# Kernel tuning notes

Hardware: AMD Instinct MI355X
Metric: run time of the kernel (lower is better)

The kernel has to match this reference:

```python
import jax, jax.numpy as jnp
import numpy as np

B, N, D = 128, 64, 20
H, WM = 256, 4
CAUG = D + 1                      # time-augmented path channels
SIG = CAUG + CAUG * (CAUG - 1) // 2   # depth-2 log-signature channels = 231
C = SIG + 1                       # time-augmented control channels = 232
EPS = 1e-5


def _ln(x, g, b):
    m = jnp.mean(x, -1, keepdims=True)
    v = jnp.var(x, -1, keepdims=True)
    return (x - m) * jax.lax.rsqrt(v + EPS) * g + b


def setup_inputs():
    key = jax.random.key(0)
    ks = jax.random.split(key, 12)
    w = lambda k, s: (jax.random.normal(k, s) * 0.02).astype(jnp.float32)
    z = lambda s: jnp.zeros(s, jnp.float32)
    o = lambda s: jnp.ones(s, jnp.float32)
    return dict(
        x=jax.random.normal(ks[0], (B, N, D), jnp.float32),
        hW1=w(ks[1], (D, H)), hb1=z(H), hW2=w(ks[2], (H, H)), hb2=z(H),
        fW1=w(ks[3], (H, WM * H)), fb1=z(WM * H), g1=o(WM * H), be1=z(WM * H),
        fW2=w(ks[4], (WM * H, H)), fb2=z(H), g2=o(H), be2=z(H),
        fW3=w(ks[5], (H, H)), fb3=z(H),
        fW4=w(ks[6], (H, H * C)), fb4=z(H * C),
        yW1=w(ks[7], (H, H // 2)), yb1=z(H // 2), yW2=w(ks[8], (H // 2, 1)), yb2=z(1),
        zW1=w(ks[9], (H, H)), zb1=z(H), zW2=w(ks[10], (H, D)), zb2=z(D),
        sg=o(SIG), sb=z(SIG),
    )


def _forward(x, hW1, hb1, hW2, hb2, fW1, fb1, g1, be1, fW2, fb2, g2, be2,
             fW3, fb3, fW4, fb4, yW1, yb1, yW2, yb2, zW1, zb1, zW2, zb2, sg, sb):
    t = jnp.linspace(0.0, 1.0, N).astype(x.dtype)
    # --- depth-2 streamed log-signature of time-augmented path, basepoint 0 ---
    p = jnp.concatenate([jnp.broadcast_to(t[None, :, None], (B, N, 1)), x], -1)  # (B,N,CAUG)
    prev = jnp.concatenate([jnp.zeros((B, 1, CAUG), x.dtype), p[:, :-1]], 1)
    d = p - prev                                          # piecewise-linear segment increments
    term = prev[..., :, None] * d[..., None, :] - d[..., :, None] * prev[..., None, :]
    levy = 0.5 * jnp.cumsum(term, axis=1)                 # Levy areas, (B,N,CAUG,CAUG)
    iu, ju = np.triu_indices(CAUG, 1)
    logsig = jnp.concatenate([p, levy[:, :, iu, ju]], -1)  # level-1 + level-2 log-sig, (B,N,SIG)
    logsig = _ln(logsig, sg, sb)                          # sig_norm
    # --- natural cubic spline of time-augmented control ---
    y = jnp.concatenate([jnp.broadcast_to(t[None, :, None], (B, N, 1)), logsig], -1)  # (B,N,C)
    h = 1.0 / (N - 1)
    A = np.zeros((N, N), np.float32)
    A[0, 0] = A[-1, -1] = 1.0
    for i in range(1, N - 1):
        A[i, i - 1] = h / 6.0
        A[i, i] = 2.0 * h / 3.0
        A[i, i + 1] = h / 6.0
    rhs = jnp.concatenate([jnp.zeros((B, 1, C), y.dtype),
                           (y[:, 2:] - 2.0 * y[:, 1:-1] + y[:, :-2]) / h,
                           jnp.zeros((B, 1, C), y.dtype)], 1)
    M = jnp.linalg.solve(jnp.asarray(A), rhs.transpose(1, 0, 2).reshape(N, B * C))
    M = M.reshape(N, B, C).transpose(1, 0, 2)             # natural-spline second derivatives
    dy = (y[:, 1:] - y[:, :-1]) / h
    d_knot = dy - (h / 6.0) * (2.0 * M[:, :-1] + M[:, 1:])   # dX/dt at left knots, (B,N-1,C)
    d_mid = dy + (h / 24.0) * (M[:, :-1] - M[:, 1:])         # dX/dt at segment midpoints
    # --- initial hidden state ---
    h0 = jax.nn.relu(x[:, 0] @ hW1 + hb1) @ hW2 + hb2

    def vf(zz):  # RDEFunc MLP -> (B,H,C)
        a = jax.nn.relu(_ln(zz @ fW1 + fb1, g1, be1))
        a = jax.nn.relu(_ln(a @ fW2 + fb2, g2, be2))
        a = jax.nn.relu(a @ fW3 + fb3)
        return (a @ fW4 + fb4).reshape(B, H, C)

    def g(zz, dX):
        return jnp.einsum('bhc,bc->bh', vf(zz), dX)

    def step(zz, dd):  # explicit midpoint step of dz = F(z) dX/dt dt
        dk, dm = dd
        k1 = g(zz, dk)
        zn = zz + h * g(zz + 0.5 * h * k1, dm)
        return zn, zn

    _, hs = jax.lax.scan(step, h0, (d_knot.transpose(1, 0, 2), d_mid.transpose(1, 0, 2)))
    hT = hs[-1]                                            # terminal hidden (return_path=False)
    Y = jax.nn.relu(hT @ yW1 + yb1) @ yW2 + yb2
    Z = jax.nn.relu(hT @ zW1 + zb1) @ zW2 + zb2
    return Y, Z, hT


def reference(x, hW1, hb1, hW2, hb2, fW1, fb1, g1, be1, fW2, fb2, g2, be2,
              fW3, fb3, fW4, fb4, yW1, yb1, yW2, yb2, zW1, zb1, zW2, zb2, sg, sb):
    return _forward(x, hW1, hb1, hW2, hb2, fW1, fb1, g1, be1, fW2, fb2, g2, be2,
                    fW3, fb3, fW4, fb4, yW1, yb1, yW2, yb2, zW1, zb1, zW2, zb2, sg, sb)
```

## Files before the change

kernel.cpp:

```cpp
#include <hip/hip_runtime.h>

#define B 128
#define N 64
#define D 20
#define H 256
#define WMH 1024
#define CAUG 21
#define SIG 231
#define C 232
#define CP 240
#define KA 288
#define NSEG 63
#define NPH 126
#define HSTEP (1.0f/63.0f)
#define EPS 1e-5f

typedef __attribute__((ext_vector_type(8))) short short8;
typedef __attribute__((ext_vector_type(4))) float f32x4;
typedef __attribute__((ext_vector_type(4))) unsigned int uint4v;
typedef unsigned int uint;

__device__ inline short f2bf(float f) {
  uint u = __float_as_uint(f);
  uint r = (u + 0x7fffu + ((u >> 16) & 1u)) >> 16;
  return (short)r;
}
__device__ inline float bf2f(short h) {
  return __uint_as_float(((uint)(unsigned short)h) << 16);
}
#define MFMA16(a, b, c) __builtin_amdgcn_mfma_f32_16x16x32_bf16((a), (b), (c), 0, 0, 0)

__device__ inline uint cloadu(const uint* p) {
  return __hip_atomic_load(p, __ATOMIC_RELAXED, __HIP_MEMORY_SCOPE_AGENT);
}
__device__ inline void cstoreu(uint* p, uint v) {
  __hip_atomic_store(p, v, __ATOMIC_RELAXED, __HIP_MEMORY_SCOPE_AGENT);
}
__device__ inline void cstoref(float* p, float v) {
  __hip_atomic_store(p, v, __ATOMIC_RELAXED, __HIP_MEMORY_SCOPE_AGENT);
}
__device__ inline int cloadi(const int* p) {
  return __hip_atomic_load(p, __ATOMIC_RELAXED, __HIP_MEMORY_SCOPE_AGENT);
}
__device__ inline void cstorei(int* p, int v) {
  __hip_atomic_store(p, v, __ATOMIC_RELAXED, __HIP_MEMORY_SCOPE_AGENT);
}

#define CLOAD8(r0,r1,r2,r3,r4,r5,r6,r7,addr)                                   \
  asm volatile("global_load_dwordx4 %0, %8, off sc0 sc1\n\t"                   \
               "global_load_dwordx4 %1, %8, off offset:16 sc0 sc1\n\t"         \
               "global_load_dwordx4 %2, %8, off offset:128 sc0 sc1\n\t"        \
               "global_load_dwordx4 %3, %8, off offset:144 sc0 sc1\n\t"        \
               "global_load_dwordx4 %4, %8, off offset:256 sc0 sc1\n\t"        \
               "global_load_dwordx4 %5, %8, off offset:272 sc0 sc1\n\t"        \
               "global_load_dwordx4 %6, %8, off offset:384 sc0 sc1\n\t"        \
               "global_load_dwordx4 %7, %8, off offset:400 sc0 sc1\n\t"        \
               "s_waitcnt vmcnt(0)"                                            \
               : "=&v"(r0), "=&v"(r1), "=&v"(r2), "=&v"(r3),                   \
                 "=&v"(r4), "=&v"(r5), "=&v"(r6), "=&v"(r7)                    \
               : "v"(addr)                                                     \
               : "memory")

#define CLOAD2(r0,r1,addr)                                                     \
  asm volatile("global_load_dwordx4 %0, %2, off sc0 sc1\n\t"                   \
               "global_load_dwordx4 %1, %2, off offset:16 sc0 sc1\n\t"         \
               "s_waitcnt vmcnt(0)"                                            \
               : "=&v"(r0), "=&v"(r1) : "v"(addr) : "memory")

#define CLOAD3A(r0,r1,r2,a0,a1,a2)                                             \
  asm volatile("global_load_dwordx4 %0, %3, off sc0 sc1\n\t"                   \
               "global_load_dwordx4 %1, %4, off sc0 sc1\n\t"                   \
               "global_load_dwordx4 %2, %5, off sc0 sc1\n\t"                   \
               "s_waitcnt vmcnt(0)"                                            \
               : "=&v"(r0), "=&v"(r1), "=&v"(r2)                               \
               : "v"(a0), "v"(a1), "v"(a2) : "memory")

__device__ inline void waitflag(const int* f, int v) {
  if (threadIdx.x == 0) {
    while (cloadi(f) < v) __builtin_amdgcn_s_sleep(2);
  }
  __builtin_amdgcn_fence(__ATOMIC_ACQUIRE, "workgroup");
  __syncthreads();
}
__device__ inline void siggroup(int* c, int nprod, int* flag) {
  __builtin_amdgcn_fence(__ATOMIC_RELEASE, "workgroup");
  __syncthreads();
  if (threadIdx.x == 0) {
    int old = __hip_atomic_fetch_add(c, 1, __ATOMIC_RELAXED, __HIP_MEMORY_SCOPE_AGENT);
    if (old == nprod - 1) cstorei(flag, 1);
  }
}

__device__ inline void unpk(uint4v a, uint4v b, short8& ah, short8& al) {
#pragma unroll
  for (int e = 0; e < 4; e++) {
    ah[e]     = (short)(a[e] >> 16); al[e]     = (short)(a[e] & 0xffffu);
    ah[4 + e] = (short)(b[e] >> 16); al[4 + e] = (short)(b[e] & 0xffffu);
  }
}

__global__ __launch_bounds__(256) void k_logsig(const float* __restrict__ x,
                                                const float* __restrict__ sg,
                                                const float* __restrict__ sb,
                                                float* __restrict__ y) {
  __shared__ float yb[N][C];
  int b = blockIdx.x, tid = threadIdx.x;
  for (int ii = tid; ii < N * CAUG; ii += 256) {
    int n = ii / CAUG, j = ii % CAUG;
    float v = (j == 0) ? (n * (1.0f / 63.0f)) : x[(b * N + n) * D + (j - 1)];
    yb[n][1 + j] = v;
  }
  __syncthreads();
  if (tid < 210) {
    int i = 0, rem = tid;
    while (rem >= (CAUG - 1) - i) { rem -= (CAUG - 1) - i; i++; }
    int j = i + 1 + rem;
    float acc = 0.f, pi_prev = 0.f, pj_prev = 0.f;
    for (int n = 0; n < N; n++) {
      float pi = yb[n][1 + i], pj = yb[n][1 + j];
      float di = pi - pi_prev, dj = pj - pj_prev;
      acc += 0.5f * (pi_prev * dj - di * pj_prev);
      yb[n][1 + CAUG + tid] = acc;
      pi_prev = pi; pj_prev = pj;
    }
  }
  __syncthreads();
  int w = tid >> 6, l = tid & 63;
  for (int n = w; n < N; n += 4) {
    float s1 = 0.f, s2 = 0.f;
    for (int s = l; s < SIG; s += 64) { float v = yb[n][1 + s]; s1 += v; s2 += v * v; }
    for (int off = 32; off > 0; off >>= 1) { s1 += __shfl_down(s1, off); s2 += __shfl_down(s2, off); }
    s1 = __shfl(s1, 0); s2 = __shfl(s2, 0);
    float mean = s1 * (1.0f / SIG);
    float var  = s2 * (1.0f / SIG) - mean * mean;
    float rs = rsqrtf(var + EPS);
    float* yrow = y + ((size_t)b * N + n) * C;
    if (l == 0) yrow[0] = n * (1.0f / 63.0f);
    for (int s = l; s < SIG; s += 64)
      yrow[1 + s] = (yb[n][1 + s] - mean) * rs * sg[s] + sb[s];
  }
}

__global__ __launch_bounds__(256) void k_spline(const float* __restrict__ y,
                                                float* __restrict__ dknot,
                                                float* __restrict__ dmid) {
  __shared__ float yb[N * C];
  __shared__ float cp_s[62], id_s[62];
  int b = blockIdx.x, tid = threadIdx.x;
  for (int ii = tid; ii < N * C; ii += 256) yb[ii] = y[(size_t)b * N * C + ii];
  if (tid == 0) {
    const float a = HSTEP / 6.f, bb = 2.f * HSTEP / 3.f;
    float id0 = 1.f / bb; id_s[0] = id0; cp_s[0] = a * id0;
    for (int j = 1; j < 62; j++) {
      float den = bb - a * cp_s[j - 1];
      float idj = 1.f / den; id_s[j] = idj; cp_s[j] = a * idj;
    }
  }
  __syncthreads();
  int c = tid;
  if (c >= 232 && c < CP) {
    for (int n = 0; n < NSEG; n++) {
      dknot[((size_t)n * B + b) * CP + c] = 0.f;
      dmid [((size_t)n * B + b) * CP + c] = 0.f;
    }
  } else if (c < 232) {
    const float a = HSTEP / 6.f;
    float dp[62];
    dp[0] = (yb[2 * C + c] - 2.f * yb[1 * C + c] + yb[0 * C + c]) * 63.0f * id_s[0];
#pragma unroll
    for (int j = 1; j < 62; j++) {
      float rj = (yb[(j + 2) * C + c] - 2.f * yb[(j + 1) * C + c] + yb[j * C + c]) * 63.0f;
      dp[j] = (rj - a * dp[j - 1]) * id_s[j];
    }
// ... 49 lines not shown
    int m = m0 + mloc;
    int hh = m / 232, cc = m - hh * 232;
    W4T[((size_t)hh * CP + cc) * KA + k0 + lane] = f2bf(tile[lane][mloc]);
  }
}

__global__ __launch_bounds__(256) void k_prep_pad(const float* __restrict__ fb4,
                                                  short* __restrict__ W4T) {
  int idx = blockIdx.x * 256 + threadIdx.x;
  const int partA = 61440 * 32;
  if (idx < partA) {
    int row = idx >> 5, j = idx & 31;
    int hh = row / CP, cc = row - hh * CP;
    short v = 0;
    if (j == 0 && cc < 232) v = f2bf(fb4[hh * 232 + cc]);
    W4T[(size_t)row * KA + 256 + j] = v;
  } else {
    int t = idx - partA;
    int k = t & 255; t >>= 8;
    int cc = 232 + (t & 7); int hh = t >> 3;
    W4T[((size_t)hh * CP + cc) * KA + k] = 0;
  }
}

__global__ __launch_bounds__(256) void k_prep_wt(const float* __restrict__ in,
                                                 short* __restrict__ out,
                                                 int K, int Nn) {
  __shared__ float tile[64][65];
  int n0 = blockIdx.x * 64, k0 = blockIdx.y * 64;
  int lane = threadIdx.x & 63, wr = threadIdx.x >> 6;
#pragma unroll
  for (int j = 0; j < 16; j++) {
    int kk = wr * 16 + j;
    tile[kk][lane] = in[(size_t)(k0 + kk) * Nn + n0 + lane];
  }
  __syncthreads();
#pragma unroll
  for (int j = 0; j < 16; j++) {
    int nl = wr * 16 + j;
    out[(size_t)(n0 + nl) * K + k0 + lane] = f2bf(tile[lane][nl]);
  }
}

__global__ __launch_bounds__(128) void k_prep_t3pad(short* __restrict__ t3aug) {
  int r = threadIdx.x;
  if (r < 128) {
    int base = ((r >> 4) * 9 + 8) * 64 + (r & 15);
#pragma unroll
    for (int q = 0; q < 4; q++)
#pragma unroll
      for (int j = 0; j < 8; j++)
        t3aug[(size_t)(base + q * 16) * 8 + j] = (q == 0 && j == 0) ? (short)0x3F80 : (short)0;
  }
}

__global__ __launch_bounds__(256) void k_prep_zero(int* __restrict__ p, int n) {
  int i = blockIdx.x * 256 + threadIdx.x;
  if (i < n) p[i] = 0;
}

__global__ __launch_bounds__(512, 1) void k_scan(
    const short* __restrict__ W1T, const float* __restrict__ fb1,
    const float* __restrict__ g1,  const float* __restrict__ be1,
    const short* __restrict__ W2T, const float* __restrict__ fb2,
    const float* __restrict__ g2,  const float* __restrict__ be2,
    const short* __restrict__ W3T, const float* __restrict__ fb3,
    const short* __restrict__ W4T,
    const float* __restrict__ dknot, const float* __restrict__ dmid,
    float* __restrict__ z, uint* __restrict__ Xu, uint* __restrict__ t3u,
    float* __restrict__ T1, float* __restrict__ T2,
    int* __restrict__ flags) {
  const int blk = blockIdx.x;
  const int tid = threadIdx.x;
  const int wave = tid >> 6, lane = tid & 63;
  const int lm = lane & 15, q = lane >> 4;
  const int m = (blk & 127) >> 4;
  const int n = blk & 15;
  const int ks = wave >> 2, nwt = wave & 3;

  __shared__ short t3s[B * KA];
  __shared__ float red2[8][256];
  __shared__ float red4[8][128];
  __shared__ float zcol[128];

  int* cS1g = flags;
  int* fS1g = flags + 1008 * 16;
  int* cS2g = flags + 2016 * 16;
  int* fS2g = flags + 3024 * 16;
  int* cS3  = flags + 4032 * 16;
  int* fS3  = flags + 4158 * 16;
  int* cS4  = flags + 4284 * 16;
  int* fS4  = flags + 4410 * 16;

  const int nts = (wave < 7) ? 2 : 1;
  const int nt0 = wave * 2;
  short8 bfr[2][9];
  for (int t = 0; t < nts; t++) {
    const short* wp = W4T + ((size_t)blk * CP + (nt0 + t) * 16 + lm) * KA + q * 8;
#pragma unroll
    for (int kc = 0; kc < 9; kc++)
      bfr[t][kc] = *(const short8*)(wp + kc * 32);
  }
  short8 w1f[4], w2f[4], w3f;
  if (blk < 128) {
    const short* p1 = W1T + ((size_t)(n * 64 + nwt * 16 + lm)) * H + ks * 128 + q * 8;
#pragma unroll
    for (int kc = 0; kc < 4; kc++) w1f[kc] = *(const short8*)(p1 + kc * 32);
    const short* p2 = W2T + ((size_t)(n * 16 + lm)) * WMH + wave * 128 + q * 8;
#pragma unroll
    for (int kc = 0; kc < 4; kc++) w2f[kc] = *(const short8*)(p2 + kc * 32);
    w3f = *(const short8*)(W3T + ((size_t)(n * 16 + lm)) * H + wave * 32 + q * 8);
  }
  if (tid < 128) zcol[tid] = z[(size_t)tid * H + blk];
  __syncthreads();

  for (int p = 0; p < NPH; p++) {
    const int seg = p >> 1, pm = p & 1;
    const float* dX = (pm ? dmid : dknot) + (size_t)seg * B * CP;
    const float scale = pm ? HSTEP : 0.5f * HSTEP;

    if (blk < 128) {
      if (p) waitflag(fS4 + (p - 1) * 16, 1);
      const uint* xp = Xu + (size_t)(m * 16 + lm) * H + ks * 128 + q * 8;
      uint4v xv[8];
      CLOAD8(xv[0], xv[1], xv[2], xv[3], xv[4], xv[5], xv[6], xv[7], xp);
      f32x4 acc = {0.f, 0.f, 0.f, 0.f};
#pragma unroll
      for (int kc = 0; kc < 4; kc++) {
        short8 ah, al;
        unpk(xv[kc * 2], xv[kc * 2 + 1], ah, al);
        acc = MFMA16(ah, w1f[kc], acc);
        acc = MFMA16(al, w1f[kc], acc);
      }
#pragma unroll
      for (int r = 0; r < 4; r++) red2[wave][(q * 4 + r) * 16 + lm] = acc[r];
      __syncthreads();
      if (wave < 4) {
        int col = n * 64 + wave * 16 + lm;
        float fb = fb1[col];
#pragma unroll
        for (int r = 0; r < 4; r++) {
          int idx = (q * 4 + r) * 16 + lm;
          float v = red2[wave][idx] + red2[wave + 4][idx] + fb;
          cstoref(T1 + (size_t)(m * 16 + q * 4 + r) * WMH + col, v);
        }
      }
      siggroup(cS1g + (m * NPH + p) * 16, 16, fS1g + (m * NPH + p) * 16);
    }

    if (blk < 128) {
      waitflag(fS1g + (m * NPH + p) * 16, 1);
      const float* tp = T1 + (size_t)(m * 16 + lm) * WMH + wave * 128 + q * 8;
      uint4v yv[8];
      CLOAD8(yv[0], yv[1], yv[2], yv[3], yv[4], yv[5], yv[6], yv[7], tp);
      float s = 0.f, ss = 0.f;
#pragma unroll
      for (int i = 0; i < 8; i++)
#pragma unroll
        for (int e = 0; e < 4; e++) {
          float v = __uint_as_float(yv[i][e]);
          s += v; ss += v * v;
        }
      s += __shfl_xor(s, 16); ss += __shfl_xor(ss, 16);
      s += __shfl_xor(s, 32); ss += __shfl_xor(ss, 32);
      if (q == 0) { red2[wave][lm] = s; red2[wave][16 + lm] = ss; }
      __syncthreads();
      float S = 0.f, SS = 0.f;
#pragma unroll
      for (int w = 0; w < 8; w++) { S += red2[w][lm]; SS += red2[w][16 + lm]; }
      float mean = S * (1.f / WMH);
      float var  = SS * (1.f / WMH) - mean * mean;
      float rsv  = rsqrtf(var + EPS);
      __syncthreads();
      f32x4 acc = {0.f, 0.f, 0.f, 0.f};
#pragma unroll
      for (int kc = 0; kc < 4; kc++) {
        int kg = wave * 128 + kc * 32 + q * 8;
        short8 ah, al;
#pragma unroll
        for (int jj = 0; jj < 8; jj++) {
          float v = __uint_as_float(yv[kc * 2 + (jj >> 2)][jj & 3]);
          float a = fmaxf((v - mean) * rsv * g1[kg + jj] + be1[kg + jj], 0.f);
          short hi = f2bf(a);
          ah[jj] = hi;
          al[jj] = f2bf(a - bf2f(hi));
        }
        acc = MFMA16(ah, w2f[kc], acc);
        acc = MFMA16(al, w2f[kc], acc);
      }
#pragma unroll
      for (int r = 0; r < 4; r++) red2[wave][(q * 4 + r) * 16 + lm] = acc[r];
      __syncthreads();
      if (tid < 256) {
        int ri = tid >> 4, ci = tid & 15;
        float v = fb2[n * 16 + ci];
#pragma unroll
        for (int w = 0; w < 8; w++) v += red2[w][tid];
        cstoref(T2 + (size_t)(m * 16 + ri) * H + n * 16 + ci, v);
      }
      siggroup(cS2g + (m * NPH + p) * 16, 16, fS2g + (m * NPH + p) * 16);
    }

    if (blk < 128) {
      waitflag(fS2g + (m * NPH + p) * 16, 1);
      const float* tp = T2 + (size_t)(m * 16 + lm) * H + wave * 32 + q * 8;
      uint4v u0, u1;
      CLOAD2(u0, u1, tp);
      float s = 0.f, ss = 0.f;
#pragma unroll
      for (int e = 0; e < 4; e++) {
        float v0 = __uint_as_float(u0[e]), v1 = __uint_as_float(u1[e]);
        s += v0 + v1; ss += v0 * v0 + v1 * v1;
      }
      s += __shfl_xor(s, 16); ss += __shfl_xor(ss, 16);
      s += __shfl_xor(s, 32); ss += __shfl_xor(ss, 32);
      if (q == 0) { red2[wave][lm] = s; red2[wave][16 + lm] = ss; }
      __syncthreads();
      float S = 0.f, SS = 0.f;
#pragma unroll
      for (int w = 0; w < 8; w++) { S += red2[w][lm]; SS += red2[w][16 + lm]; }
      float mean = S * (1.f / H);
      float var  = SS * (1.f / H) - mean * mean;
      float rsv  = rsqrtf(var + EPS);
      __syncthreads();
      int kg = wave * 32 + q * 8;
      short8 ah, al;
#pragma unroll
      for (int jj = 0; jj < 8; jj++) {
        float v = __uint_as_float((jj < 4 ? u0[jj & 3] : u1[jj & 3]));
        float a = fmaxf((v - mean) * rsv * g2[kg + jj] + be2[kg + jj], 0.f);
        short hi = f2bf(a);
        ah[jj] = hi;
        al[jj] = f2bf(a - bf2f(hi));
      }
      f32x4 acc = {0.f, 0.f, 0.f, 0.f};
      acc = MFMA16(ah, w3f, acc);
      acc = MFMA16(al, w3f, acc);
#pragma unroll
      for (int r = 0; r < 4; r++) red2[wave][(q * 4 + r) * 16 + lm] = acc[r];
      __syncthreads();
      if (tid < 256) {
        int ri = tid >> 4, ci = tid & 15;
        float v = fb3[n * 16 + ci];
#pragma unroll
        for (int w = 0; w < 8; w++) v += red2[w][tid];
        v = fmaxf(v, 0.f);
        float vo = __shfl_xor(v, 1);
        if ((ci & 1) == 0) {
          int kglob = n * 16 + ci;
          int d = (m * 9 + (kglob >> 5)) * 64 + ((kglob >> 3) & 3) * 16 + ri;
          uint u = ((uint)(unsigned short)f2bf(vo) << 16)
                 | (unsigned short)f2bf(v);
          cstoreu(t3u + d * 4 + ((kglob & 7) >> 1), u);
        }
      }
      siggroup(cS3 + p * 16, 128, fS3 + p * 16);
    }

    {
      waitflag(fS3 + p * 16, 1);
#pragma unroll
      for (int g = 0; g < 3; g++) {
        const uint* a0 = t3u + (g * 3 + 0) * 2048 + tid * 4;
        const uint* a1 = t3u + (g * 3 + 1) * 2048 + tid * 4;
        const uint* a2 = t3u + (g * 3 + 2) * 2048 + tid * 4;
        uint4v r0, r1, r2;
        CLOAD3A(r0, r1, r2, a0, a1, a2);
        *(uint4v*)(t3s + (size_t)((g * 3 + 0) * 2048 + tid * 4) * 2) = r0;
        *(uint4v*)(t3s + (size_t)((g * 3 + 1) * 2048 + tid * 4) * 2) = r1;
        *(uint4v*)(t3s + (size_t)((g * 3 + 2) * 2048 + tid * 4) * 2) = r2;
      }
      __syncthreads();
      for (int mm = 0; mm < 8; mm++) {
        short8 afr[9];
#pragma unroll
        for (int kc = 0; kc < 9; kc++)
          afr[kc] = *(const short8*)(t3s + (size_t)((mm * 9 + kc) * 64 + lane) * 8);
        f32x4 acc0 = {0.f, 0.f, 0.f, 0.f}, acc1 = {0.f, 0.f, 0.f, 0.f};
#pragma unroll
        for (int kc = 0; kc < 9; kc++) {
          acc0 = MFMA16(afr[kc], bfr[0][kc], acc0);
          if (nts > 1) acc1 = MFMA16(afr[kc], bfr[1][kc], acc1);
        }
        float part[4];
#pragma unroll
        for (int r = 0; r < 4; r++) {
          int row = mm * 16 + q * 4 + r;
          float pv = acc0[r] * dX[(size_t)row * CP + nt0 * 16 + lm];
          if (nts > 1) pv += acc1[r] * dX[(size_t)row * CP + (nt0 + 1) * 16 + lm];
          part[r] = pv;
        }
#pragma unroll
        for (int r = 0; r < 4; r++) {
          part[r] += __shfl_xor(part[r], 1);
          part[r] += __shfl_xor(part[r], 2);
          part[r] += __shfl_xor(part[r], 4);
          part[r] += __shfl_xor(part[r], 8);
        }
        if (lm == 0) {
#pragma unroll
          for (int r = 0; r < 4; r++) red4[wave][mm * 16 + q * 4 + r] = part[r];
        }
      }
      __syncthreads();
      if (tid < 128) {
        int row = tid;
        float s = 0.f;
#pragma unroll
        for (int w = 0; w < 8; w++) s += red4[w][row];
        float zo = zcol[row] + scale * s;
        if (pm) zcol[row] = zo;
        if (p == NPH - 1) z[(size_t)row * H + blk] = zo;
        short hi = f2bf(zo);
        short lo = f2bf(zo - bf2f(hi));
        cstoreu(Xu + (size_t)row * H + blk,
                ((uint)(unsigned short)hi << 16) | (unsigned short)lo);
      }
      siggroup(cS4 + p * 16, 256, fS4 + p * 16);
    }
  }
}

__global__ __launch_bounds__(256) void k_final(const float* __restrict__ z,
    const float* __restrict__ yW1, const float* __restrict__ yb1,
    const float* __restrict__ yW2, const float* __restrict__ yb2,
    const float* __restrict__ zW1, const float* __restrict__ zb1,
    const float* __restrict__ zW2, const float* __restrict__ zb2,
    float* __restrict__ out) {
  __shared__ float ht[H];
  __shared__ float ry[128];
  __shared__ float rz[H];
  int b = blockIdx.x, tid = threadIdx.x;
  ht[tid] = z[(size_t)b * H + tid];
  __syncthreads();
  if (tid < 128) {
    float s = yb1[tid];
    for (int k = 0; k < H; k++) s += ht[k] * yW1[k * 128 + tid];
    ry[tid] = fmaxf(s, 0.f);
  }
  {
    float s = zb1[tid];
    for (int k = 0; k < H; k++) s += ht[k] * zW1[k * H + tid];
    rz[tid] = fmaxf(s, 0.f);
  }
  __syncthreads();
  if (tid < 64) {
    float sv = ry[tid] * yW2[tid] + ry[tid + 64] * yW2[tid + 64];
    for (int off = 32; off > 0; off >>= 1) sv += __shfl_down(sv, off);
    if (tid == 0) out[b] = sv + yb2[0];
  }
  if (tid < D) {
    float s = zb2[tid];
    for (int k = 0; k < H; k++) s += rz[k] * zW2[k * D + tid];
    out[B + b * D + tid] = s;
  }
  out[B + B * D + (size_t)b * H + tid] = ht[tid];
}

extern "C" void kernel_launch(void* const* d_in, const int* in_sizes, int n_in,
                              void* d_out, int out_size, void* d_ws, size_t ws_size,
                              hipStream_t stream) {
  const float* x   = (const float*)d_in[0];
  const float* hW1 = (const float*)d_in[1];
  const float* hb1 = (const float*)d_in[2];
  const float* hW2 = (const float*)d_in[3];
  const float* hb2 = (const float*)d_in[4];
  const float* fW1 = (const float*)d_in[5];
  const float* fb1 = (const float*)d_in[6];
  const float* g1  = (const float*)d_in[7];
  const float* be1 = (const float*)d_in[8];
  const float* fW2 = (const float*)d_in[9];
  const float* fb2 = (const float*)d_in[10];
  const float* g2  = (const float*)d_in[11];
  const float* be2 = (const float*)d_in[12];
  const float* fW3 = (const float*)d_in[13];
  const float* fb3 = (const float*)d_in[14];
  const float* fW4 = (const float*)d_in[15];
  const float* fb4 = (const float*)d_in[16];
  const float* yW1 = (const float*)d_in[17];
  const float* yb1 = (const float*)d_in[18];
  const float* yW2 = (const float*)d_in[19];
  const float* yb2 = (const float*)d_in[20];
  const float* zW1 = (const float*)d_in[21];
  const float* zb1 = (const float*)d_in[22];
  const float* zW2 = (const float*)d_in[23];
  const float* zb2 = (const float*)d_in[24];
  const float* sg  = (const float*)d_in[25];
  const float* sb  = (const float*)d_in[26];

  float* ws     = (float*)d_ws;
  float* dknot  = ws;
  float* dmid   = dknot + (size_t)NSEG * B * CP;
  float* z      = dmid + (size_t)NSEG * B * CP;
  float* T1     = z + B * H;
  float* T2     = T1 + B * WMH;
  uint* Xu      = (uint*)(T2 + B * H);
  uint* t3u     = Xu + B * H;
  int* flags    = (int*)(t3u + B * KA / 2);
  short* w1T    = (short*)(flags + 72576);
  short* w2T    = w1T + H * WMH;
  short* w3T    = w2T + H * WMH;
  short* W4T    = w3T + H * H;
  float* y      = (float*)W4T;

  hipLaunchKernelGGL(k_logsig, dim3(B), dim3(256), 0, stream, x, sg, sb, y);
  hipLaunchKernelGGL(k_spline, dim3(B), dim3(256), 0, stream, y, dknot, dmid);
  hipLaunchKernelGGL(k_h0,     dim3(B), dim3(256), 0, stream, x, hW1, hb1, hW2, hb2, z, Xu);
  hipLaunchKernelGGL(k_prep_t,   dim3(928, 4), dim3(256), 0, stream, fW4, W4T);
  hipLaunchKernelGGL(k_prep_pad, dim3(9728),   dim3(256), 0, stream, fb4, W4T);
  hipLaunchKernelGGL(k_prep_wt,  dim3(16, 4),  dim3(256), 0, stream, fW1, w1T, H, WMH);
  hipLaunchKernelGGL(k_prep_wt,  dim3(4, 16),  dim3(256), 0, stream, fW2, w2T, WMH, H);
  hipLaunchKernelGGL(k_prep_wt,  dim3(4, 4),   dim3(256), 0, stream, fW3, w3T, H, H);
  hipLaunchKernelGGL(k_prep_t3pad, dim3(1), dim3(128), 0, stream, (short*)t3u);
  hipLaunchKernelGGL(k_prep_zero, dim3(284), dim3(256), 0, stream, flags, 72576);

  void* args[] = {
    (void*)&w1T, (void*)&fb1, (void*)&g1, (void*)&be1,
    (void*)&w2T, (void*)&fb2, (void*)&g2, (void*)&be2,
    (void*)&w3T, (void*)&fb3, (void*)&W4T,
    (void*)&dknot, (void*)&dmid,
    (void*)&z, (void*)&Xu, (void*)&t3u,
    (void*)&T1, (void*)&T2, (void*)&flags
  };
  hipLaunchCooperativeKernel((const void*)k_scan, dim3(256), dim3(512), args, 0, stream);

  hipLaunchKernelGGL(k_final, dim3(B), dim3(256), 0, stream, z,
                     yW1, yb1, yW2, yb2, zW1, zb1, zW2, zb2, (float*)d_out);
}
```

Baseline: 4.563 ms.

## Replace cache-bypassing asm loads with plain loads plus agent-scope acquire fence

Drops the inline-asm sc0 sc1 global loads used to read cross-block intermediates (X, T1, T2, t3) and uses ordinary vector loads instead. An agent-scope acquire fence on the first wave in waitflag is meant to keep them coherent. It also caches LayerNorm gamma/beta and bias vectors in shared memory and issues all nine t3 loads at once instead of three batches. The plain loads can be scheduled and overlapped by the compiler and may hit cache, but correctness now depends on the acquire fence invalidating stale cached lines on every wave's reads.

```diff
diff --git a/kernel.cpp b/kernel.cpp
--- a/kernel.cpp
+++ b/kernel.cpp
@@ -30,9 +30,6 @@
 }
 #define MFMA16(a, b, c) __builtin_amdgcn_mfma_f32_16x16x32_bf16((a), (b), (c), 0, 0, 0)
 
-__device__ inline uint cloadu(const uint* p) {
-  return __hip_atomic_load(p, __ATOMIC_RELAXED, __HIP_MEMORY_SCOPE_AGENT);
-}
 __device__ inline void cstoreu(uint* p, uint v) {
   __hip_atomic_store(p, v, __ATOMIC_RELAXED, __HIP_MEMORY_SCOPE_AGENT);
 }
@@ -46,40 +43,13 @@
   __hip_atomic_store(p, v, __ATOMIC_RELAXED, __HIP_MEMORY_SCOPE_AGENT);
 }
 
-#define CLOAD8(r0,r1,r2,r3,r4,r5,r6,r7,addr)                                   \
-  asm volatile("global_load_dwordx4 %0, %8, off sc0 sc1\n\t"                   \
-               "global_load_dwordx4 %1, %8, off offset:16 sc0 sc1\n\t"         \
-               "global_load_dwordx4 %2, %8, off offset:128 sc0 sc1\n\t"        \
-               "global_load_dwordx4 %3, %8, off offset:144 sc0 sc1\n\t"        \
-               "global_load_dwordx4 %4, %8, off offset:256 sc0 sc1\n\t"        \
-               "global_load_dwordx4 %5, %8, off offset:272 sc0 sc1\n\t"        \
-               "global_load_dwordx4 %6, %8, off offset:384 sc0 sc1\n\t"        \
-               "global_load_dwordx4 %7, %8, off offset:400 sc0 sc1\n\t"        \
-               "s_waitcnt vmcnt(0)"                                            \
-               : "=&v"(r0), "=&v"(r1), "=&v"(r2), "=&v"(r3),                   \
-                 "=&v"(r4), "=&v"(r5), "=&v"(r6), "=&v"(r7)                    \
-               : "v"(addr)                                                     \
-               : "memory")
-
-#define CLOAD2(r0,r1,addr)                                                     \
-  asm volatile("global_load_dwordx4 %0, %2, off sc0 sc1\n\t"                   \
-               "global_load_dwordx4 %1, %2, off offset:16 sc0 sc1\n\t"         \
-               "s_waitcnt vmcnt(0)"                                            \
-               : "=&v"(r0), "=&v"(r1) : "v"(addr) : "memory")
-
-#define CLOAD3A(r0,r1,r2,a0,a1,a2)                                             \
-  asm volatile("global_load_dwordx4 %0, %3, off sc0 sc1\n\t"                   \
-               "global_load_dwordx4 %1, %4, off sc0 sc1\n\t"                   \
-               "global_load_dwordx4 %2, %5, off sc0 sc1\n\t"                   \
-               "s_waitcnt vmcnt(0)"                                            \
-               : "=&v"(r0), "=&v"(r1), "=&v"(r2)                               \
-               : "v"(a0), "v"(a1), "v"(a2) : "memory")
-
 __device__ inline void waitflag(const int* f, int v) {
-  if (threadIdx.x == 0) {
-    while (cloadi(f) < v) __builtin_amdgcn_s_sleep(2);
-  }
-  __builtin_amdgcn_fence(__ATOMIC_ACQUIRE, "workgroup");
+  if (threadIdx.x < 64) {
+    if (threadIdx.x == 0) {
+      while (cloadi(f) < v) __builtin_amdgcn_s_sleep(2);
+    }
+    __builtin_amdgcn_fence(__ATOMIC_ACQUIRE, "agent");
+  }
   __syncthreads();
 }
 __device__ inline void siggroup(int* c, int nprod, int* flag) {
@@ -304,6 +274,10 @@
   __shared__ float red2[8][256];
   __shared__ float red4[8][128];
   __shared__ float zcol[128];
+  __shared__ float g1s[WMH], be1s[WMH];
+  __shared__ float g2s[H], be2s[H];
+  __shared__ float fb1s[64];
+  __shared__ float fb2s[16], fb3s[16];
 
   int* cS1g = flags;
   int* fS1g = flags + 1008 * 16;
@@ -333,9 +307,14 @@
     for (int kc = 0; kc < 4; kc++) w2f[kc] = *(const short8*)(p2 + kc * 32);
     w3f = *(const short8*)(W3T + ((size_t)(n * 16 + lm)) * H + wave * 32 + q * 8);
   }
+  for (int i = tid; i < WMH; i += 512) { g1s[i] = g1[i]; be1s[i] = be1[i]; }
+  for (int i = tid; i < H; i += 512)   { g2s[i] = g2[i]; be2s[i] = be2[i]; }
+  if (tid < 64) fb1s[tid] = fb1[n * 64 + tid];
+  if (tid < 16) { fb2s[tid] = fb2[n * 16 + tid]; fb3s[tid] = fb3[n * 16 + tid]; }
   if (tid < 128) zcol[tid] = z[(size_t)tid * H + blk];
   __syncthreads();
 
+#pragma unroll 1
   for (int p = 0; p < NPH; p++) {
     const int seg = p >> 1, pm = p & 1;
     const float* dX = (pm ? dmid : dknot) + (size_t)seg * B * CP;
@@ -345,7 +324,14 @@
       if (p) waitflag(fS4 + (p - 1) * 16, 1);
       const uint* xp = Xu + (size_t)(m * 16 + lm) * H + ks * 128 + q * 8;
       uint4v xv[8];
-      CLOAD8(xv[0], xv[1], xv[2], xv[3], xv[4], xv[5], xv[6], xv[7], xp);
+      xv[0] = *(const uint4v*)(xp);
+      xv[1] = *(const uint4v*)(xp + 4);
+      xv[2] = *(const uint4v*)(xp + 32);
+      xv[3] = *(const uint4v*)(xp + 36);
+      xv[4] = *(const uint4v*)(xp + 64);
+      xv[5] = *(const uint4v*)(xp + 68);
+      xv[6] = *(const uint4v*)(xp + 96);
+      xv[7] = *(const uint4v*)(xp + 100);
       f32x4 acc = {0.f, 0.f, 0.f, 0.f};
 #pragma unroll
       for (int kc = 0; kc < 4; kc++) {
@@ -359,7 +345,7 @@
       __syncthreads();
       if (wave < 4) {
         int col = n * 64 + wave * 16 + lm;
-        float fb = fb1[col];
+        float fb = fb1s[wave * 16 + lm];
 #pragma unroll
         for (int r = 0; r < 4; r++) {
           int idx = (q * 4 + r) * 16 + lm;
@@ -373,14 +359,21 @@
     if (blk < 128) {
       waitflag(fS1g + (m * NPH + p) * 16, 1);
       const float* tp = T1 + (size_t)(m * 16 + lm) * WMH + wave * 128 + q * 8;
-      uint4v yv[8];
-      CLOAD8(yv[0], yv[1], yv[2], yv[3], yv[4], yv[5], yv[6], yv[7], tp);
+      f32x4 yv[8];
+      yv[0] = *(const f32x4*)(tp);
+      yv[1] = *(const f32x4*)(tp + 4);
+      yv[2] = *(const f32x4*)(tp + 32);
+      yv[3] = *(const f32x4*)(tp + 36);
+      yv[4] = *(const f32x4*)(tp + 64);
+      yv[5] = *(const f32x4*)(tp + 68);
+      yv[6] = *(const f32x4*)(tp + 96);
+      yv[7] = *(const f32x4*)(tp + 100);
       float s = 0.f, ss = 0.f;
 #pragma unroll
       for (int i = 0; i < 8; i++)
 #pragma unroll
         for (int e = 0; e < 4; e++) {
-          float v = __uint_as_float(yv[i][e]);
+          float v = yv[i][e];
           s += v; ss += v * v;
         }
       s += __shfl_xor(s, 16); ss += __shfl_xor(ss, 16);
@@ -401,8 +394,8 @@
         short8 ah, al;
 #pragma unroll
         for (int jj = 0; jj < 8; jj++) {
-          float v = __uint_as_float(yv[kc * 2 + (jj >> 2)][jj & 3]);
-          float a = fmaxf((v - mean) * rsv * g1[kg + jj] + be1[kg + jj], 0.f);
+          float v = yv[kc * 2 + (jj >> 2)][jj & 3];
+          float a = fmaxf((v - mean) * rsv * g1s[kg + jj] + be1s[kg + jj], 0.f);
           short hi = f2bf(a);
           ah[jj] = hi;
           al[jj] = f2bf(a - bf2f(hi));
@@ -415,7 +408,7 @@
       __syncthreads();
       if (tid < 256) {
         int ri = tid >> 4, ci = tid & 15;
-        float v = fb2[n * 16 + ci];
+        float v = fb2s[ci];
 #pragma unroll
         for (int w = 0; w < 8; w++) v += red2[w][tid];
         cstoref(T2 + (size_t)(m * 16 + ri) * H + n * 16 + ci, v);
@@ -426,12 +419,12 @@
     if (blk < 128) {
       waitflag(fS2g + (m * NPH + p) * 16, 1);
       const float* tp = T2 + (size_t)(m * 16 + lm) * H + wave * 32 + q * 8;
-      uint4v u0, u1;
-      CLOAD2(u0, u1, tp);
+      f32x4 u0 = *(const f32x4*)(tp);
+      f32x4 u1 = *(const f32x4*)(tp + 4);
       float s = 0.f, ss = 0.f;
 #pragma unroll
       for (int e = 0; e < 4; e++) {
-        float v0 = __uint_as_float(u0[e]), v1 = __uint_as_float(u1[e]);
+        float v0 = u0[e], v1 = u1[e];
         s += v0 + v1; ss += v0 * v0 + v1 * v1;
       }
       s += __shfl_xor(s, 16); ss += __shfl_xor(ss, 16);
@@ -449,8 +442,8 @@
       short8 ah, al;
 #pragma unroll
       for (int jj = 0; jj < 8; jj++) {
-        float v = __uint_as_float((jj < 4 ? u0[jj & 3] : u1[jj & 3]));
-        float a = fmaxf((v - mean) * rsv * g2[kg + jj] + be2[kg + jj], 0.f);
+        float v = (jj < 4 ? u0[jj & 3] : u1[jj & 3]);
+        float a = fmaxf((v - mean) * rsv * g2s[kg + jj] + be2s[kg + jj], 0.f);
         short hi = f2bf(a);
         ah[jj] = hi;
         al[jj] = f2bf(a - bf2f(hi));
@@ -463,7 +456,7 @@
       __syncthreads();
       if (tid < 256) {
         int ri = tid >> 4, ci = tid & 15;
-        float v = fb3[n * 16 + ci];
+        float v = fb3s[ci];
 #pragma unroll
         for (int w = 0; w < 8; w++) v += red2[w][tid];
         v = fmaxf(v, 0.f);
@@ -481,16 +474,26 @@
 
     {
       waitflag(fS3 + p * 16, 1);
-#pragma unroll
-      for (int g = 0; g < 3; g++) {
-        const uint* a0 = t3u + (g * 3 + 0) * 2048 + tid * 4;
-        const uint* a1 = t3u + (g * 3 + 1) * 2048 + tid * 4;
-        const uint* a2 = t3u + (g * 3 + 2) * 2048 + tid * 4;
-        uint4v r0, r1, r2;
-        CLOAD3A(r0, r1, r2, a0, a1, a2);
-        *(uint4v*)(t3s + (size_t)((g * 3 + 0) * 2048 + tid * 4) * 2) = r0;
-        *(uint4v*)(t3s + (size_t)((g * 3 + 1) * 2048 + tid * 4) * 2) = r1;
-        *(uint4v*)(t3s + (size_t)((g * 3 + 2) * 2048 + tid * 4) * 2) = r2;
+      {
+        const uint* tb = t3u + tid * 4;
+        uint4v r0 = *(const uint4v*)(tb);
+        uint4v r1 = *(const uint4v*)(tb + 2048);
+        uint4v r2 = *(const uint4v*)(tb + 4096);
+        uint4v r3 = *(const uint4v*)(tb + 6144);
+        uint4v r4 = *(const uint4v*)(tb + 8192);
+        uint4v r5 = *(const uint4v*)(tb + 10240);
+        uint4v r6 = *(const uint4v*)(tb + 12288);
+        uint4v r7 = *(const uint4v*)(tb + 14336);
+        uint4v r8 = *(const uint4v*)(tb + 16384);
+        *(uint4v*)(t3s + (size_t)(0 * 2048 + tid * 4) * 2) = r0;
+        *(uint4v*)(t3s + (size_t)(1 * 2048 + tid * 4) * 2) = r1;
+        *(uint4v*)(t3s + (size_t)(2 * 2048 + tid * 4) * 2) = r2;
+        *(uint4v*)(t3s + (size_t)(3 * 2048 + tid * 4) * 2) = r3;
+        *(uint4v*)(t3s + (size_t)(4 * 2048 + tid * 4) * 2) = r4;
+        *(uint4v*)(t3s + (size_t)(5 * 2048 + tid * 4) * 2) = r5;
+        *(uint4v*)(t3s + (size_t)(6 * 2048 + tid * 4) * 2) = r6;
+        *(uint4v*)(t3s + (size_t)(7 * 2048 + tid * 4) * 2) = r7;
+        *(uint4v*)(t3s + (size_t)(8 * 2048 + tid * 4) * 2) = r8;
       }
       __syncthreads();
       for (int mm = 0; mm < 8; mm++) {
```

New measurement: 4.842 ms. +6.1%, slower.

## Replace atomic counter barriers with per-block epoch flags polled by a wavefront

Applied to the files above, without the earlier changes.

Inter-block synchronisation in the persistent cooperative scan kernel changes from atomic fetch-add counters plus a completion flag to per-producer epoch flags. Each block posts its phase number, and consumers poll all producer flags in parallel with one wavefront using a vector load and __all. This removes the serialised atomic round trip, avoids the extra hop through a second flag, and shrinks the flag array that has to be zeroed. It also caches the layernorm gains and biases in LDS and merges the t3 staging into a single batch of nine loads. The cost is heavier polling traffic on the flag lines and more shared memory per block.

```diff
diff --git a/kernel.cpp b/kernel.cpp
--- a/kernel.cpp
+++ b/kernel.cpp
@@ -18,6 +18,8 @@
 typedef __attribute__((ext_vector_type(8))) short short8;
 typedef __attribute__((ext_vector_type(4))) float f32x4;
 typedef __attribute__((ext_vector_type(4))) unsigned int uint4v;
+typedef __attribute__((ext_vector_type(2))) int int2v;
+typedef __attribute__((ext_vector_type(4))) int int4v;
 typedef unsigned int uint;
 
 __device__ inline short f2bf(float f) {
@@ -30,17 +32,11 @@
 }
 #define MFMA16(a, b, c) __builtin_amdgcn_mfma_f32_16x16x32_bf16((a), (b), (c), 0, 0, 0)
 
-__device__ inline uint cloadu(const uint* p) {
-  return __hip_atomic_load(p, __ATOMIC_RELAXED, __HIP_MEMORY_SCOPE_AGENT);
-}
 __device__ inline void cstoreu(uint* p, uint v) {
   __hip_atomic_store(p, v, __ATOMIC_RELAXED, __HIP_MEMORY_SCOPE_AGENT);
 }
 __device__ inline void cstoref(float* p, float v) {
   __hip_atomic_store(p, v, __ATOMIC_RELAXED, __HIP_MEMORY_SCOPE_AGENT);
-}
-__device__ inline int cloadi(const int* p) {
-  return __hip_atomic_load(p, __ATOMIC_RELAXED, __HIP_MEMORY_SCOPE_AGENT);
 }
 __device__ inline void cstorei(int* p, int v) {
   __hip_atomic_store(p, v, __ATOMIC_RELAXED, __HIP_MEMORY_SCOPE_AGENT);
@@ -67,28 +63,69 @@
                "s_waitcnt vmcnt(0)"                                            \
                : "=&v"(r0), "=&v"(r1) : "v"(addr) : "memory")
 
-#define CLOAD3A(r0,r1,r2,a0,a1,a2)                                             \
-  asm volatile("global_load_dwordx4 %0, %3, off sc0 sc1\n\t"                   \
-               "global_load_dwordx4 %1, %4, off sc0 sc1\n\t"                   \
-               "global_load_dwordx4 %2, %5, off sc0 sc1\n\t"                   \
+#define CLOAD9(r0,r1,r2,r3,r4,r5,r6,r7,r8,a0,a1,a2,a3,a4,a5,a6,a7,a8)          \
+  asm volatile("global_load_dwordx4 %0, %9, off sc0 sc1\n\t"                   \
+               "global_load_dwordx4 %1, %10, off sc0 sc1\n\t"                  \
+               "global_load_dwordx4 %2, %11, off sc0 sc1\n\t"                  \
+               "global_load_dwordx4 %3, %12, off sc0 sc1\n\t"                  \
+               "global_load_dwordx4 %4, %13, off sc0 sc1\n\t"                  \
+               "global_load_dwordx4 %5, %14, off sc0 sc1\n\t"                  \
+               "global_load_dwordx4 %6, %15, off sc0 sc1\n\t"                  \
+               "global_load_dwordx4 %7, %16, off sc0 sc1\n\t"                  \
+               "global_load_dwordx4 %8, %17, off sc0 sc1\n\t"                  \
                "s_waitcnt vmcnt(0)"                                            \
-               : "=&v"(r0), "=&v"(r1), "=&v"(r2)                               \
-               : "v"(a0), "v"(a1), "v"(a2) : "memory")
-
-__device__ inline void waitflag(const int* f, int v) {
-  if (threadIdx.x == 0) {
-    while (cloadi(f) < v) __builtin_amdgcn_s_sleep(2);
+               : "=&v"(r0), "=&v"(r1), "=&v"(r2), "=&v"(r3), "=&v"(r4),        \
+                 "=&v"(r5), "=&v"(r6), "=&v"(r7), "=&v"(r8)                    \
+               : "v"(a0), "v"(a1), "v"(a2), "v"(a3), "v"(a4), "v"(a5),         \
+                 "v"(a6), "v"(a7), "v"(a8)                                     \
+               : "memory")
+
+__device__ inline void post(int* w, int v) {
+  __builtin_amdgcn_fence(__ATOMIC_RELEASE, "workgroup");
+  __syncthreads();
+  if (threadIdx.x == 0) cstorei(w, v);
+}
+__device__ inline void poll16(const int* f, int tgt) {
+  if (threadIdx.x < 64) {
+    const int* p = f + (threadIdx.x & 15);
+    for (;;) {
+      int v;
+      asm volatile("global_load_dword %0, %1, off sc0 sc1\n\ts_waitcnt vmcnt(0)"
+                   : "=v"(v) : "v"(p) : "memory");
+      if (__all(v >= tgt)) break;
+      __builtin_amdgcn_s_sleep(1);
+    }
   }
   __builtin_amdgcn_fence(__ATOMIC_ACQUIRE, "workgroup");
   __syncthreads();
 }
-__device__ inline void siggroup(int* c, int nprod, int* flag) {
-  __builtin_amdgcn_fence(__ATOMIC_RELEASE, "workgroup");
-  __syncthreads();
-  if (threadIdx.x == 0) {
-    int old = __hip_atomic_fetch_add(c, 1, __ATOMIC_RELAXED, __HIP_MEMORY_SCOPE_AGENT);
-    if (old == nprod - 1) cstorei(flag, 1);
-  }
+__device__ inline void poll128(const int* f, int tgt) {
+  if (threadIdx.x < 64) {
+    const int* p = f + threadIdx.x * 2;
+    for (;;) {
+      int2v v;
+      asm volatile("global_load_dwordx2 %0, %1, off sc0 sc1\n\ts_waitcnt vmcnt(0)"
+                   : "=v"(v) : "v"(p) : "memory");
+      if (__all(v[0] >= tgt && v[1] >= tgt)) break;
+      __builtin_amdgcn_s_sleep(1);
+    }
+  }
+  __builtin_amdgcn_fence(__ATOMIC_ACQUIRE, "workgroup");
+  __syncthreads();
+}
+__device__ inline void poll256(const int* f, int tgt) {
+  if (threadIdx.x < 64) {
+    const int* p = f + threadIdx.x * 4;
+    for (;;) {
+      int4v v;
+      asm volatile("global_load_dwordx4 %0, %1, off sc0 sc1\n\ts_waitcnt vmcnt(0)"
+                   : "=v"(v) : "v"(p) : "memory");
+      if (__all(v[0] >= tgt && v[1] >= tgt && v[2] >= tgt && v[3] >= tgt)) break;
+      __builtin_amdgcn_s_sleep(1);
+    }
+  }
+  __builtin_amdgcn_fence(__ATOMIC_ACQUIRE, "workgroup");
+  __syncthreads();
 }
 
 __device__ inline void unpk(uint4v a, uint4v b, short8& ah, short8& al) {
@@ -304,15 +341,15 @@
   __shared__ float red2[8][256];
   __shared__ float red4[8][128];
   __shared__ float zcol[128];
-
-  int* cS1g = flags;
-  int* fS1g = flags + 1008 * 16;
-  int* cS2g = flags + 2016 * 16;
-  int* fS2g = flags + 3024 * 16;
-  int* cS3  = flags + 4032 * 16;
-  int* fS3  = flags + 4158 * 16;
-  int* cS4  = flags + 4284 * 16;
-  int* fS4  = flags + 4410 * 16;
+  __shared__ float g1s[WMH], be1s[WMH];
+  __shared__ float g2s[H], be2s[H];
+  __shared__ float fb1s[64];
+  __shared__ float fb2s[16], fb3s[16];
+
+  int* eS1 = flags;
+  int* eS2 = flags + 128;
+  int* eS3 = flags + 256;
+  int* eS4 = flags + 384;
 
   const int nts = (wave < 7) ? 2 : 1;
   const int nt0 = wave * 2;
@@ -333,33 +370,40 @@
     for (int kc = 0; kc < 4; kc++) w2f[kc] = *(const short8*)(p2 + kc * 32);
     w3f = *(const short8*)(W3T + ((size_t)(n * 16 + lm)) * H + wave * 32 + q * 8);
   }
+  for (int i = tid; i < WMH; i += 512) { g1s[i] = g1[i]; be1s[i] = be1[i]; }
+  for (int i = tid; i < H; i += 512)   { g2s[i] = g2[i]; be2s[i] = be2[i]; }
+  if (tid < 64) fb1s[tid] = fb1[n * 64 + tid];
+  if (tid < 16) { fb2s[tid] = fb2[n * 16 + tid]; fb3s[tid] = fb3[n * 16 + tid]; }
   if (tid < 128) zcol[tid] = z[(size_t)tid * H + blk];
   __syncthreads();
 
+#pragma unroll 1
   for (int p = 0; p < NPH; p++) {
     const int seg = p >> 1, pm = p & 1;
     const float* dX = (pm ? dmid : dknot) + (size_t)seg * B * CP;
     const float scale = pm ? HSTEP : 0.5f * HSTEP;
 
     if (blk < 128) {
-      if (p) waitflag(fS4 + (p - 1) * 16, 1);
+      if (p) poll256(eS4, p);
       const uint* xp = Xu + (size_t)(m * 16 + lm) * H + ks * 128 + q * 8;
       uint4v xv[8];
       CLOAD8(xv[0], xv[1], xv[2], xv[3], xv[4], xv[5], xv[6], xv[7], xp);
-      f32x4 acc = {0.f, 0.f, 0.f, 0.f};
-#pragma unroll
-      for (int kc = 0; kc < 4; kc++) {
-        short8 ah, al;
-        unpk(xv[kc * 2], xv[kc * 2 + 1], ah, al);
-        acc = MFMA16(ah, w1f[kc], acc);
-        acc = MFMA16(al, w1f[kc], acc);
-      }
-#pragma unroll
-      for (int r = 0; r < 4; r++) red2[wave][(q * 4 + r) * 16 + lm] = acc[r];
+      {
+        f32x4 acc = {0.f, 0.f, 0.f, 0.f};
+#pragma unroll
+        for (int kc = 0; kc < 4; kc++) {
+          short8 ah, al;
+          unpk(xv[kc * 2], xv[kc * 2 + 1], ah, al);
+          acc = MFMA16(ah, w1f[kc], acc);
+          acc = MFMA16(al, w1f[kc], acc);
+        }
+#pragma unroll
+        for (int r = 0; r < 4; r++) red2[wave][(q * 4 + r) * 16 + lm] = acc[r];
+      }
       __syncthreads();
       if (wave < 4) {
         int col = n * 64 + wave * 16 + lm;
-        float fb = fb1[col];
+        float fb = fb1s[wave * 16 + lm];
 #pragma unroll
         for (int r = 0; r < 4; r++) {
           int idx = (q * 4 + r) * 16 + lm;
@@ -367,103 +411,103 @@
           cstoref(T1 + (size_t)(m * 16 + q * 4 + r) * WMH + col, v);
         }
       }
-      siggroup(cS1g + (m * NPH + p) * 16, 16, fS1g + (m * NPH + p) * 16);
-    }
-
-    if (blk < 128) {
-      waitflag(fS1g + (m * NPH + p) * 16, 1);
+      post(eS1 + m * 16 + n, p + 1);
+
+      poll16(eS1 + m * 16, p + 1);
       const float* tp = T1 + (size_t)(m * 16 + lm) * WMH + wave * 128 + q * 8;
       uint4v yv[8];
       CLOAD8(yv[0], yv[1], yv[2], yv[3], yv[4], yv[5], yv[6], yv[7], tp);
-      float s = 0.f, ss = 0.f;
-#pragma unroll
-      for (int i = 0; i < 8; i++)
+      {
+        float s = 0.f, ss = 0.f;
+#pragma unroll
+        for (int i = 0; i < 8; i++)
+#pragma unroll
+          for (int e = 0; e < 4; e++) {
+            float v = __uint_as_float(yv[i][e]);
+            s += v; ss += v * v;
+          }
+        s += __shfl_xor(s, 16); ss += __shfl_xor(ss, 16);
+        s += __shfl_xor(s, 32); ss += __shfl_xor(ss, 32);
+        if (q == 0) { red2[wave][lm] = s; red2[wave][16 + lm] = ss; }
+        __syncthreads();
+        float S = 0.f, SS = 0.f;
+#pragma unroll
+        for (int w = 0; w < 8; w++) { S += red2[w][lm]; SS += red2[w][16 + lm]; }
+        float mean = S * (1.f / WMH);
+        float var  = SS * (1.f / WMH) - mean * mean;
+        float rsv  = rsqrtf(var + EPS);
+        __syncthreads();
+        f32x4 acc = {0.f, 0.f, 0.f, 0.f};
+#pragma unroll
+        for (int kc = 0; kc < 4; kc++) {
+          int kg = wave * 128 + kc * 32 + q * 8;
+          short8 ah, al;
+#pragma unroll
+          for (int jj = 0; jj < 8; jj++) {
+            float v = __uint_as_float(yv[kc * 2 + (jj >> 2)][jj & 3]);
+            float a = fmaxf((v - mean) * rsv * g1s[kg + jj] + be1s[kg + jj], 0.f);
+            short hi = f2bf(a);
+            ah[jj] = hi;
+            al[jj] = f2bf(a - bf2f(hi));
+          }
+          acc = MFMA16(ah, w2f[kc], acc);
+          acc = MFMA16(al, w2f[kc], acc);
+        }
+#pragma unroll
+        for (int r = 0; r < 4; r++) red2[wave][(q * 4 + r) * 16 + lm] = acc[r];
+      }
+      __syncthreads();
+      if (tid < 256) {
+        int ri = tid >> 4, ci = tid & 15;
+        float v = fb2s[ci];
+#pragma unroll
+        for (int w = 0; w < 8; w++) v += red2[w][tid];
+        cstoref(T2 + (size_t)(m * 16 + ri) * H + n * 16 + ci, v);
+      }
+      post(eS2 + m * 16 + n, p + 1);
+
+      poll16(eS2 + m * 16, p + 1);
+      const float* t2p = T2 + (size_t)(m * 16 + lm) * H + wave * 32 + q * 8;
+      uint4v u0, u1;
+      CLOAD2(u0, u1, t2p);
+      {
+        float s = 0.f, ss = 0.f;
 #pragma unroll
         for (int e = 0; e < 4; e++) {
-          float v = __uint_as_float(yv[i][e]);
-          s += v; ss += v * v;
-        }
-      s += __shfl_xor(s, 16); ss += __shfl_xor(ss, 16);
-      s += __shfl_xor(s, 32); ss += __shfl_xor(ss, 32);
-      if (q == 0) { red2[wave][lm] = s; red2[wave][16 + lm] = ss; }
-      __syncthreads();
-      float S = 0.f, SS = 0.f;
-#pragma unroll
-      for (int w = 0; w < 8; w++) { S += red2[w][lm]; SS += red2[w][16 + lm]; }
-      float mean = S * (1.f / WMH);
-      float var  = SS * (1.f / WMH) - mean * mean;
-      float rsv  = rsqrtf(var + EPS);
-      __syncthreads();
-      f32x4 acc = {0.f, 0.f, 0.f, 0.f};
-#pragma unroll
-      for (int kc = 0; kc < 4; kc++) {
-        int kg = wave * 128 + kc * 32 + q * 8;
+          float v0 = __uint_as_float(u0[e]), v1 = __uint_as_float(u1[e]);
+          s += v0 + v1; ss += v0 * v0 + v1 * v1;
+        }
+        s += __shfl_xor(s, 16); ss += __shfl_xor(ss, 16);
+        s += __shfl_xor(s, 32); ss += __shfl_xor(ss, 32);
+        if (q == 0) { red2[wave][lm] = s; red2[wave][16 + lm] = ss; }
+        __syncthreads();
+        float S = 0.f, SS = 0.f;
+#pragma unroll
+        for (int w = 0; w < 8; w++) { S += red2[w][lm]; SS += red2[w][16 + lm]; }
+        float mean = S * (1.f / H);
+        float var  = SS * (1.f / H) - mean * mean;
+        float rsv  = rsqrtf(var + EPS);
+        __syncthreads();
+        int kg = wave * 32 + q * 8;
         short8 ah, al;
 #pragma unroll
         for (int jj = 0; jj < 8; jj++) {
-          float v = __uint_as_float(yv[kc * 2 + (jj >> 2)][jj & 3]);
-          float a = fmaxf((v - mean) * rsv * g1[kg + jj] + be1[kg + jj], 0.f);
+          float v = __uint_as_float((jj < 4 ? u0[jj & 3] : u1[jj & 3]));
+          float a = fmaxf((v - mean) * rsv * g2s[kg + jj] + be2s[kg + jj], 0.f);
           short hi = f2bf(a);
           ah[jj] = hi;
           al[jj] = f2bf(a - bf2f(hi));
         }
-        acc = MFMA16(ah, w2f[kc], acc);
-        acc = MFMA16(al, w2f[kc], acc);
-      }
-#pragma unroll
-      for (int r = 0; r < 4; r++) red2[wave][(q * 4 + r) * 16 + lm] = acc[r];
+        f32x4 acc = {0.f, 0.f, 0.f, 0.f};
+        acc = MFMA16(ah, w3f, acc);
+        acc = MFMA16(al, w3f, acc);
+#pragma unroll
+        for (int r = 0; r < 4; r++) red2[wave][(q * 4 + r) * 16 + lm] = acc[r];
+      }
       __syncthreads();
       if (tid < 256) {
         int ri = tid >> 4, ci = tid & 15;
-        float v = fb2[n * 16 + ci];
-#pragma unroll
-        for (int w = 0; w < 8; w++) v += red2[w][tid];
-        cstoref(T2 + (size_t)(m * 16 + ri) * H + n * 16 + ci, v);
-      }
-      siggroup(cS2g + (m * NPH + p) * 16, 16, fS2g + (m * NPH + p) * 16);
-    }
-
-    if (blk < 128) {
-      waitflag(fS2g + (m * NPH + p) * 16, 1);
-      const float* tp = T2 + (size_t)(m * 16 + lm) * H + wave * 32 + q * 8;
-      uint4v u0, u1;
-      CLOAD2(u0, u1, tp);
-      float s = 0.f, ss = 0.f;
-#pragma unroll
-      for (int e = 0; e < 4; e++) {
-        float v0 = __uint_as_float(u0[e]), v1 = __uint_as_float(u1[e]);
-        s += v0 + v1; ss += v0 * v0 + v1 * v1;
-      }
-      s += __shfl_xor(s, 16); ss += __shfl_xor(ss, 16);
-      s += __shfl_xor(s, 32); ss += __shfl_xor(ss, 32);
-      if (q == 0) { red2[wave][lm] = s; red2[wave][16 + lm] = ss; }
-      __syncthreads();
-      float S = 0.f, SS = 0.f;
-#pragma unroll
-      for (int w = 0; w < 8; w++) { S += red2[w][lm]; SS += red2[w][16 + lm]; }
-      float mean = S * (1.f / H);
-      float var  = SS * (1.f / H) - mean * mean;
-      float rsv  = rsqrtf(var + EPS);
-      __syncthreads();
-      int kg = wave * 32 + q * 8;
-      short8 ah, al;
-#pragma unroll
-      for (int jj = 0; jj < 8; jj++) {
-        float v = __uint_as_float((jj < 4 ? u0[jj & 3] : u1[jj & 3]));
-        float a = fmaxf((v - mean) * rsv * g2[kg + jj] + be2[kg + jj], 0.f);
-        short hi = f2bf(a);
-        ah[jj] = hi;
-        al[jj] = f2bf(a - bf2f(hi));
-      }
-      f32x4 acc = {0.f, 0.f, 0.f, 0.f};
-      acc = MFMA16(ah, w3f, acc);
-      acc = MFMA16(al, w3f, acc);
-#pragma unroll
-      for (int r = 0; r < 4; r++) red2[wave][(q * 4 + r) * 16 + lm] = acc[r];
-      __syncthreads();
-      if (tid < 256) {
-        int ri = tid >> 4, ci = tid & 15;
-        float v = fb3[n * 16 + ci];
+        float v = fb3s[ci];
 #pragma unroll
         for (int w = 0; w < 8; w++) v += red2[w][tid];
         v = fmaxf(v, 0.f);
@@ -476,21 +520,26 @@
           cstoreu(t3u + d * 4 + ((kglob & 7) >> 1), u);
         }
       }
-      siggroup(cS3 + p * 16, 128, fS3 + p * 16);
+      post(eS3 + m * 16 + n, p + 1);
     }
 
     {
-      waitflag(fS3 + p * 16, 1);
-#pragma unroll
-      for (int g = 0; g < 3; g++) {
-        const uint* a0 = t3u + (g * 3 + 0) * 2048 + tid * 4;
-        const uint* a1 = t3u + (g * 3 + 1) * 2048 + tid * 4;
-        const uint* a2 = t3u + (g * 3 + 2) * 2048 + tid * 4;
-        uint4v r0, r1, r2;
-        CLOAD3A(r0, r1, r2, a0, a1, a2);
-        *(uint4v*)(t3s + (size_t)((g * 3 + 0) * 2048 + tid * 4) * 2) = r0;
-        *(uint4v*)(t3s + (size_t)((g * 3 + 1) * 2048 + tid * 4) * 2) = r1;
-        *(uint4v*)(t3s + (size_t)((g * 3 + 2) * 2048 + tid * 4) * 2) = r2;
+      poll128(eS3, p + 1);
+      {
+        const uint* tb = t3u + tid * 4;
+        uint4v r0, r1, r2, r3, r4, r5, r6, r7, r8;
+        CLOAD9(r0, r1, r2, r3, r4, r5, r6, r7, r8,
+               tb, tb + 2048, tb + 4096, tb + 6144, tb + 8192,
+               tb + 10240, tb + 12288, tb + 14336, tb + 16384);
+        *(uint4v*)(t3s + (size_t)(0 * 2048 + tid * 4) * 2) = r0;
+        *(uint4v*)(t3s + (size_t)(1 * 2048 + tid * 4) * 2) = r1;
+        *(uint4v*)(t3s + (size_t)(2 * 2048 + tid * 4) * 2) = r2;
+        *(uint4v*)(t3s + (size_t)(3 * 2048 + tid * 4) * 2) = r3;
+        *(uint4v*)(t3s + (size_t)(4 * 2048 + tid * 4) * 2) = r4;
+        *(uint4v*)(t3s + (size_t)(5 * 2048 + tid * 4) * 2) = r5;
+        *(uint4v*)(t3s + (size_t)(6 * 2048 + tid * 4) * 2) = r6;
+        *(uint4v*)(t3s + (size_t)(7 * 2048 + tid * 4) * 2) = r7;
+        *(uint4v*)(t3s + (size_t)(8 * 2048 + tid * 4) * 2) = r8;
       }
       __syncthreads();
       for (int mm = 0; mm < 8; mm++) {
@@ -538,7 +587,7 @@
         cstoreu(Xu + (size_t)row * H + blk,
                 ((uint)(unsigned short)hi << 16) | (unsigned short)lo);
       }
-      siggroup(cS4 + p * 16, 256, fS4 + p * 16);
+      post(eS4 + blk, p + 1);
     }
   }
 }
@@ -619,7 +668,7 @@
   uint* Xu      = (uint*)(T2 + B * H);
   uint* t3u     = Xu + B * H;
   int* flags    = (int*)(t3u + B * KA / 2);
-  short* w1T    = (short*)(flags + 72576);
+  short* w1T    = (short*)(flags + 1024);
   short* w2T    = w1T + H * WMH;
   short* w3T    = w2T + H * WMH;
   short* W4T    = w3T + H * H;
@@ -634,7 +683,7 @@
   hipLaunchKernelGGL(k_prep_wt,  dim3(4, 16),  dim3(256), 0, stream, fW2, w2T, WMH, H);
   hipLaunchKernelGGL(k_prep_wt,  dim3(4, 4),   dim3(256), 0, stream, fW3, w3T, H, H);
   hipLaunchKernelGGL(k_prep_t3pad, dim3(1), dim3(128), 0, stream, (short*)t3u);
-  hipLaunchKernelGGL(k_prep_zero, dim3(284), dim3(256), 0, stream, flags, 72576);
+  hipLaunchKernelGGL(k_prep_zero, dim3(4), dim3(256), 0, stream, flags, 1024);
 
   void* args[] = {
     (void*)&w1T, (void*)&fb1, (void*)&g1, (void*)&be1,
```

Result: no change. 4.611 ms (+1.0%).
